# Kernel optimization log

Measured on AMD Instinct MI355X. Metric: run time of the kernel, lower is better.

Reference implementation:

```python
import jax, jax.numpy as jnp
import numpy as np

MAX_DISP = 40   # init kwarg max_disp
STRIDE_2 = 1    # init kwarg stride_2


def setup_inputs() -> dict:
    key = jax.random.key(0)
    k1, k2 = jax.random.split(key)
    B, C, H, W = 8, 128, 160, 320
    x_1 = jax.random.normal(k1, (B, C, H, W), dtype=jnp.float32)
    x_2 = jax.random.normal(k2, (B, C, H, W), dtype=jnp.float32)
    return {"x_1": x_1, "x_2": x_2}


def reference(x_1, x_2):
    # x_1, x_2: [B, C, H, W]
    pad = MAX_DISP * 2
    W = x_1.shape[3]
    # left-pad x_2 along width, matching F.pad(x_2, (pad, 0, 0, 0))
    x2p = jnp.pad(x_2, ((0, 0), (0, 0), (0, 0), (pad, 0)))
    # one [B,H,W] correlation map per displacement (small fixed set of 81 shifts)
    outs = [
        jnp.sum(x_1 * jax.lax.dynamic_slice_in_dim(x2p, d, W, axis=3), axis=1)
        for d in range(0, pad + 1, STRIDE_2)
    ]
    return jnp.stack(outs, axis=1)  # [B, D, H, W], D = 2*max_disp//stride + 1
```

## Files before the change

kernel.cpp:

```cpp
#include <hip/hip_runtime.h>


#define CB 8
#define CC 128
#define CH 160
#define CW 320
#define CD 81
#define CPAD 80
#define TW 160
#define NTHR 640
#define AROWS 160
#define BROWS 240
#define KC 64
#define ROWP 72
#define HW (CH*CW)

typedef __attribute__((ext_vector_type(8))) short short8;
typedef __attribute__((ext_vector_type(4))) float f32x4;

__device__ __forceinline__ unsigned pk2(float a, float b) {
    unsigned ua = __float_as_uint(a), ub = __float_as_uint(b);
    ua = (ua + 0x7fffu + ((ua >> 16) & 1u)) >> 16;
    ub = (ub + 0x7fffu + ((ub >> 16) & 1u)) >> 16;
    return ua | (ub << 16);
}

__global__ __launch_bounds__(NTHR, 5) void corr1d_mfma(
    const float* __restrict__ x1,
    const float* __restrict__ x2,
    float* __restrict__ out)
{
    __shared__ __align__(16) unsigned short lA[AROWS * ROWP];
    __shared__ __align__(16) unsigned short lB[BROWS * ROWP];

    const int tid = threadIdx.x;
    const int bid = blockIdx.x;
    const int wt = bid & 1;
    const int h  = (bid >> 1) % CH;
    const int b  = bid / (2 * CH);
    const int w0 = wt * TW;

    const int lane = tid & 63;
    const int s    = tid >> 6;
    const int n    = lane & 15;
    const int q    = lane >> 4;

    const float* x1p = x1 + ((size_t)b * CC * CH + (size_t)h) * CW;
    const float* x2p = x2 + ((size_t)b * CC * CH + (size_t)h) * CW;

    f32x4 acc[6];
#pragma unroll
    for (int t = 0; t < 6; t++) acc[t] = (f32x4){0.f, 0.f, 0.f, 0.f};

    for (int c0 = 0; c0 < CC; c0 += KC) {
        if (c0) __syncthreads();

#pragma unroll
        for (int j = 0; j < 3; j++) {
            int i = tid + j * NTHR;
            if (i < 1600) {
                int cq = i & 15;
                int rt = i >> 4;
                int kl = cq << 2;
                int c  = c0 + kl;
                float4 v[4];
                unsigned short* dst;
                if (rt < 40) {
                    int gw = w0 + (rt << 2);
                    const float* p = x1p + (size_t)c * HW + gw;
#pragma unroll
                    for (int cc = 0; cc < 4; cc++)
                        v[cc] = *(const float4*)(p + (size_t)cc * HW);
                    dst = &lA[(rt << 2) * ROWP + kl];
                } else {
                    int rb = rt - 40;
                    int gw = w0 - CPAD + (rb << 2);
                    if (gw >= 0) {
                        const float* p = x2p + (size_t)c * HW + gw;
#pragma unroll
                        for (int cc = 0; cc < 4; cc++)
                            v[cc] = *(const float4*)(p + (size_t)cc * HW);
                    } else {
#pragma unroll
                        for (int cc = 0; cc < 4; cc++)
                            v[cc] = make_float4(0.f, 0.f, 0.f, 0.f);
                    }
                    dst = &lB[(rb << 2) * ROWP + kl];
                }
                uint2 r0 = make_uint2(pk2(v[0].x, v[1].x), pk2(v[2].x, v[3].x));
                uint2 r1 = make_uint2(pk2(v[0].y, v[1].y), pk2(v[2].y, v[3].y));
                uint2 r2 = make_uint2(pk2(v[0].z, v[1].z), pk2(v[2].z, v[3].z));
                uint2 r3 = make_uint2(pk2(v[0].w, v[1].w), pk2(v[2].w, v[3].w));
                *(uint2*)(dst + 0 * ROWP) = r0;
                *(uint2*)(dst + 1 * ROWP) = r1;
                *(uint2*)(dst + 2 * ROWP) = r2;
                *(uint2*)(dst + 3 * ROWP) = r3;
            }
        }
        __syncthreads();

        const unsigned short* arow = &lA[(16 * s + n) * ROWP];
#pragma unroll
        for (int ko = 0; ko < KC; ko += 32) {
            short8 av = *(const short8*)(arow + ko + 8 * q);
#pragma unroll
            for (int t = 0; t < 6; t++) {
                short8 bv = *(const short8*)(&lB[(16 * (s + t) + n) * ROWP + ko + 8 * q]);
                acc[t] = __builtin_amdgcn_mfma_f32_16x16x32_bf16(av, bv, acc[t], 0, 0, 0);
            }
        }
    }

    float* op = out + ((size_t)b * CD * CH + (size_t)h) * CW + w0 + 16 * s;
#pragma unroll
    for (int t = 0; t < 6; t++) {
#pragma unroll
        for (int r = 0; r < 4; r++) {
            int m = 4 * q + r;
            int d = 16 * t + n - m;
            if (d >= 0 && d <= CPAD)
                op[(size_t)d * HW + m] = acc[t][r];
        }
    }
}

extern "C" void kernel_launch(void* const* d_in, const int* in_sizes, int n_in,
                              void* d_out, int out_size, void* d_ws, size_t ws_size,
                              hipStream_t stream) {
    const float* x1 = (const float*)d_in[0];
    const float* x2 = (const float*)d_in[1];
    float* out = (float*)d_out;
    dim3 grid(CB * CH * 2);
    dim3 block(NTHR);
    corr1d_mfma<<<grid, block, 0, stream>>>(x1, x2, out);
}
```

Before: 510.0 us.

## Shrink correlation tiles and stage output through LDS for vectorized stores

Halves the width tile to 80 columns with 320-thread blocks and 32-channel K chunks, which doubles the grid and raises the occupancy hint. The LDS is reused after the MFMA loop as an output staging buffer, so results are written to global memory as coalesced float4 rows per displacement instead of scattered scalar stores. In exchange, the x2 halo is reloaded more often relative to useful work (160 B rows per 80 outputs), and there are more K iterations with barriers plus an extra LDS round trip for the output.

```diff
diff --git a/kernel.cpp b/kernel.cpp
--- a/kernel.cpp
+++ b/kernel.cpp
@@ -7,13 +7,15 @@
 #define CW 320
 #define CD 81
 #define CPAD 80
-#define TW 160
-#define NTHR 640
-#define AROWS 160
-#define BROWS 240
-#define KC 64
-#define ROWP 72
+#define TW 80
+#define NTHR 320
+#define AROWS 80
+#define BROWS 160
+#define KC 32
+#define ROWP 40
+#define OSTRIDE 81
 #define HW (CH*CW)
+#define SMEM_BYTES 26368
 
 typedef __attribute__((ext_vector_type(8))) short short8;
 typedef __attribute__((ext_vector_type(4))) float f32x4;
@@ -25,19 +27,20 @@
     return ua | (ub << 16);
 }
 
-__global__ __launch_bounds__(NTHR, 5) void corr1d_mfma(
+__global__ __launch_bounds__(NTHR, 8) void corr1d_mfma3(
     const float* __restrict__ x1,
     const float* __restrict__ x2,
     float* __restrict__ out)
 {
-    __shared__ __align__(16) unsigned short lA[AROWS * ROWP];
-    __shared__ __align__(16) unsigned short lB[BROWS * ROWP];
+    __shared__ __align__(16) char smem[SMEM_BYTES];
+    unsigned short* lds = (unsigned short*)smem;
+    float* obuf = (float*)smem;
 
     const int tid = threadIdx.x;
     const int bid = blockIdx.x;
-    const int wt = bid & 1;
-    const int h  = (bid >> 1) % CH;
-    const int b  = bid / (2 * CH);
+    const int wt = bid & 3;
+    const int h  = (bid >> 2) % CH;
+    const int b  = bid / (4 * CH);
     const int w0 = wt * TW;
 
     const int lane = tid & 63;
@@ -56,24 +59,23 @@
         if (c0) __syncthreads();
 
 #pragma unroll
-        for (int j = 0; j < 3; j++) {
-            int i = tid + j * NTHR;
-            if (i < 1600) {
-                int cq = i & 15;
-                int rt = i >> 4;
+        for (int ii = 0; ii < 2; ii++) {
+            int i = tid + ii * NTHR;
+            if (i < 480) {
+                int cq = i & 7;
+                int rt = i >> 3;
                 int kl = cq << 2;
                 int c  = c0 + kl;
                 float4 v[4];
                 unsigned short* dst;
-                if (rt < 40) {
-                    int gw = w0 + (rt << 2);
-                    const float* p = x1p + (size_t)c * HW + gw;
+                if (rt < 20) {
+                    const float* p = x1p + (size_t)c * HW + w0 + (rt << 2);
 #pragma unroll
                     for (int cc = 0; cc < 4; cc++)
                         v[cc] = *(const float4*)(p + (size_t)cc * HW);
-                    dst = &lA[(rt << 2) * ROWP + kl];
+                    dst = lds + (rt << 2) * ROWP + kl;
                 } else {
-                    int rb = rt - 40;
+                    int rb = rt - 20;
                     int gw = w0 - CPAD + (rb << 2);
                     if (gw >= 0) {
                         const float* p = x2p + (size_t)c * HW + gw;
@@ -85,7 +87,7 @@
                         for (int cc = 0; cc < 4; cc++)
                             v[cc] = make_float4(0.f, 0.f, 0.f, 0.f);
                     }
-                    dst = &lB[(rb << 2) * ROWP + kl];
+                    dst = lds + (AROWS + (rb << 2)) * ROWP + kl;
                 }
                 uint2 r0 = make_uint2(pk2(v[0].x, v[1].x), pk2(v[2].x, v[3].x));
                 uint2 r1 = make_uint2(pk2(v[0].y, v[1].y), pk2(v[2].y, v[3].y));
@@ -99,19 +101,15 @@
         }
         __syncthreads();
 
-        const unsigned short* arow = &lA[(16 * s + n) * ROWP];
+        short8 av = *(const short8*)(lds + (16 * s + n) * ROWP + 8 * q);
 #pragma unroll
-        for (int ko = 0; ko < KC; ko += 32) {
-            short8 av = *(const short8*)(arow + ko + 8 * q);
-#pragma unroll
-            for (int t = 0; t < 6; t++) {
-                short8 bv = *(const short8*)(&lB[(16 * (s + t) + n) * ROWP + ko + 8 * q]);
-                acc[t] = __builtin_amdgcn_mfma_f32_16x16x32_bf16(av, bv, acc[t], 0, 0, 0);
-            }
+        for (int t = 0; t < 6; t++) {
+            short8 bv = *(const short8*)(lds + (AROWS + 16 * (s + t) + n) * ROWP + 8 * q);
+            acc[t] = __builtin_amdgcn_mfma_f32_16x16x32_bf16(av, bv, acc[t], 0, 0, 0);
         }
     }
+    __syncthreads();
 
-    float* op = out + ((size_t)b * CD * CH + (size_t)h) * CW + w0 + 16 * s;
 #pragma unroll
     for (int t = 0; t < 6; t++) {
 #pragma unroll
@@ -119,8 +117,18 @@
             int m = 4 * q + r;
             int d = 16 * t + n - m;
             if (d >= 0 && d <= CPAD)
-                op[(size_t)d * HW + m] = acc[t][r];
+                obuf[d * OSTRIDE + 16 * s + m] = acc[t][r];
         }
+    }
+    __syncthreads();
+
+    float* op = out + ((size_t)b * CD * CH + (size_t)h) * CW + w0;
+    for (int i = tid; i < CD * (TW / 4); i += NTHR) {
+        int d  = i / (TW / 4);
+        int wq = i - d * (TW / 4);
+        const float* r0 = obuf + d * OSTRIDE + 4 * wq;
+        float4 v = make_float4(r0[0], r0[1], r0[2], r0[3]);
+        *(float4*)(op + (size_t)d * HW + 4 * wq) = v;
     }
 }
 
@@ -130,7 +138,7 @@
     const float* x1 = (const float*)d_in[0];
     const float* x2 = (const float*)d_in[1];
     float* out = (float*)d_out;
-    dim3 grid(CB * CH * 2);
+    dim3 grid(CB * CH * 4);
     dim3 block(NTHR);
-    corr1d_mfma<<<grid, block, 0, stream>>>(x1, x2, out);
+    corr1d_mfma3<<<grid, block, 0, stream>>>(x1, x2, out);
 }
```

Result: no change. 516.9 us (+1.4%).
